# Performance work log

Measured on AMD Instinct MI355X. Metric: run time of the kernel, lower is better.

Reference implementation:

```python
import jax, jax.numpy as jnp
import numpy as np

MUL_S, MUL_V = 16, 8   # 16x0e + 8x1o -> input dim 16 + 8*3 = 40
N = 500_000
SQRT3 = 3.0 ** 0.5

# e3nn normalize2mom: scale act so E[act(x)^2]=1 for x~N(0,1)
def _norm2mom(act):
    xs = np.linspace(-12.0, 12.0, 200001)
    pdf = np.exp(-0.5 * xs * xs) / np.sqrt(2.0 * np.pi)
    m2 = np.trapz(act(xs) ** 2 * pdf, xs)
    return float(1.0 / np.sqrt(m2))

SILU_C = _norm2mom(lambda x: x / (1.0 + np.exp(-x)))
SIG_C = _norm2mom(lambda x: 1.0 / (1.0 + np.exp(-x)))

# e3nn path normalization (irrep_normalization='component', path_normalization='element')
C_SC = (1.0 / (MUL_S * MUL_S + MUL_V * MUL_V)) ** 0.5          # 0e outputs (scalars & gates)
C_V = (3.0 / (2 * MUL_S * MUL_V)) ** 0.5                        # 1o output (gated)


def setup_inputs() -> dict:
    key = jax.random.key(0)
    ks = jax.random.split(key, 7)
    return {
        "x": jax.random.normal(ks[0], (N, MUL_S + 3 * MUL_V), dtype=jnp.float32),
        "W_ss0": jax.random.normal(ks[1], (MUL_S, MUL_S, MUL_S), dtype=jnp.float32),
        "W_vv0": jax.random.normal(ks[2], (MUL_V, MUL_V, MUL_S), dtype=jnp.float32),
        "W_ss1": jax.random.normal(ks[3], (MUL_S, MUL_S, MUL_V), dtype=jnp.float32),
        "W_vv1": jax.random.normal(ks[4], (MUL_V, MUL_V, MUL_V), dtype=jnp.float32),
        "W_sv": jax.random.normal(ks[5], (MUL_S, MUL_V, MUL_V), dtype=jnp.float32),
        "W_vs": jax.random.normal(ks[6], (MUL_V, MUL_S, MUL_V), dtype=jnp.float32),
    }


def reference(x, W_ss0, W_vv0, W_ss1, W_vv1, W_sv, W_vs):
    # split irreps: scalars [N,16], vectors [N,8,3]
    s = x[:, :MUL_S]
    v = x[:, MUL_S:].reshape(-1, MUL_V, 3)

    # FullyConnectedTensorProduct(x, x) -> scalars(16x0e) + gates(8x0e) + gated(8x1o)
    # wigner_3j(0,0,0)=1 ; (1,1,0)=(0,1,1)=(1,0,1)=I/sqrt(3)
    scal = C_SC * (
        jnp.einsum('zu,zv,uvw->zw', s, s, W_ss0)
        + jnp.einsum('zui,zvi,uvw->zw', v, v, W_vv0) / SQRT3
    )
    gates_pre = C_SC * (
        jnp.einsum('zu,zv,uvw->zw', s, s, W_ss1)
        + jnp.einsum('zui,zvi,uvw->zw', v, v, W_vv1) / SQRT3
    )
    gated = (C_V / SQRT3) * (
        jnp.einsum('zu,zvi,uvw->zwi', s, v, W_sv)
        + jnp.einsum('zui,zv,uvw->zwi', v, s, W_vs)
    )

    # Gate: normalized silu on even scalars, normalized sigmoid gates * gated vectors
    out_s = SILU_C * jax.nn.silu(scal)                 # [N,16]
    g = SIG_C * jax.nn.sigmoid(gates_pre)              # [N,8]
    out_v = g[:, :, None] * gated                      # [N,8,3]
    return jnp.concatenate([out_s, out_v.reshape(-1, MUL_V * 3)], axis=1)
```

## Files before the change

kernel.cpp:

```cpp
#include <hip/hip_runtime.h>
#include <math.h>

#define NPTS 200001

typedef _Float16 f16;
typedef f16 f16x2 __attribute__((ext_vector_type(2)));
typedef f16 f16x8 __attribute__((ext_vector_type(8)));
typedef float f32x16 __attribute__((ext_vector_type(16)));

#define B1BYTES  21952
#define B2OFF    21952
#define BBYTES   24128
#define STAGEOFF 24128
#define LDSBYTES (24128 + 4*2560)

__global__ void prep(const float* __restrict__ wss0, const float* __restrict__ wvv0,
                     const float* __restrict__ wss1, const float* __restrict__ wvv1,
                     const float* __restrict__ wsv,  const float* __restrict__ wvs,
                     float* __restrict__ partials, f16* __restrict__ bpack)
{
    const int b = blockIdx.x;
    const int t = threadIdx.x;
    if (b < 4) {
        float ls = 0.f, lg = 0.f;
        for (int i = b * 256 + t; i < NPTS; i += 1024) {
            float xv  = -12.0f + 24.0f * ((float)i / 200000.0f);
            float pdf = __expf(-0.5f * xv * xv) * 0.39894228040143267794f;
            float sg  = 1.0f / (1.0f + __expf(-xv));
            float si  = xv * sg;
            float wt  = (i == 0 || i == NPTS - 1) ? 0.5f : 1.0f;
            ls = fmaf(wt * si * si, pdf, ls);
            lg = fmaf(wt * sg * sg, pdf, lg);
        }
        __shared__ float r1[256], r2[256];
        r1[t] = ls; r2[t] = lg;
        __syncthreads();
        for (int st = 128; st > 0; st >>= 1) {
            if (t < st) { r1[t] += r1[t + st]; r2[t] += r2[t + st]; }
            __syncthreads();
        }
        if (t == 0) { partials[b] = r1[0]; partials[4 + b] = r2[0]; }
    } else {
        const int gid = (b - 4) * 256 + t;
        const float CSC  = 0.05590169943749474241f;
        const float CSC3 = 0.05590169943749474241f / 1.7320508075688772935f;
        if (gid < 10976) {
            const int tk   = gid / 392;
            const int rem  = gid - tk * 392;
            const int unit = rem >> 3;
            const int j    = rem & 7;
            float val = 0.f;
            if (unit < 48) {
                const int hf  = (unit >= 24) ? 1 : 0;
                const int col = unit - 24 * hf;
                const int k   = tk * 16 + hf * 8 + j;
                if (k < 256) {
                    const int u = k >> 4, t16 = k & 15;
                    val = (col < 16) ? CSC * wss0[(u * 16 + t16) * 16 + col]
                                     : CSC * wss1[(u * 16 + t16) * 8 + (col - 16)];
                } else {
                    const int kk = k - 256;
                    const int r8 = (kk >> 3) & 7, c8 = kk & 7;
                    val = (col < 16) ? CSC3 * wvv0[(r8 * 8 + c8) * 16 + col]
                                     : CSC3 * wvv1[(r8 * 8 + c8) * 8 + (col - 16)];
                }
            }
            bpack[gid] = (f16)val;
        } else if (gid < 12064) {
            const int e    = gid - 10976;
            const int ks   = e / 136;
            const int rem  = e - ks * 136;
            const int unit = rem >> 3;
            const int j    = rem & 7;
            float val = 0.f;
            if (unit < 16) {
                const int hf = unit >> 3;
                const int w  = unit & 7;
                const int k  = ks * 16 + hf * 8 + j;
                const int a  = k >> 3, bb = k & 7;
                val = 0.0625f * (wsv[(a * 8 + bb) * 8 + w] + wvs[(bb * 16 + a) * 8 + w]);
            }
            bpack[gid] = (f16)val;
        }
    }
}

__global__ __launch_bounds__(256, 4) void seg_main(
    const float* __restrict__ x,
    const f16* __restrict__ bpack,
    const float* __restrict__ partials,
    float* __restrict__ out, int n, int nchunks)
{
    const int tid  = threadIdx.x;
    const int lane = tid & 63;
    const int wid  = tid >> 6;
    const int col  = lane & 31;
    const int hf   = lane >> 5;

    __shared__ float4 lds4[LDSBYTES / 16];
    {
        const float4* src = (const float4*)bpack;
#pragma unroll
        for (int i = 0; i < 6; ++i) {
            const int idx = i * 256 + tid;
            if (idx < BBYTES / 16) lds4[idx] = src[idx];
        }
    }
    __syncthreads();

    char* ldsc = (char*)lds4;
    const int uA = (col < 24) ? (hf * 24 + col) * 16 : 48 * 16;
    const int u0 = B2OFF + ((col >= 24) ? (hf * 8 + col - 24) * 16 : 256);
    const int u1 = B2OFF + ((col < 8)   ? (hf * 8 + col) * 16      : 256);
    const int u2 = B2OFF + ((col >= 8 && col < 16) ? (hf * 8 + col - 8) * 16 : 256);
    const f16x8* BA  = (const f16x8*)(ldsc + uA);
    const f16x8* B0p = (const f16x8*)(ldsc + u0);
    const f16x8* B1p = (const f16x8*)(ldsc + u1);
    const f16x8* B2p = (const f16x8*)(ldsc + u2);

    float*  stagef = (float*)(ldsc + STAGEOFF + wid * 2560);
    float4* stage4 = (float4*)(ldsc + STAGEOFF + wid * 2560);

    const int gsrc = 4 * (hf * 32 + 16 + (col & 7));
    const int vo   = 16 + (col & 7) * 3 + ((col < 8) ? 1 : ((col < 16) ? 2 : 0));
    const bool wrV = (col < 16) || (col >= 24);

    const float dx = 24.0f / 200000.0f;
    const float silu_c = rsqrtf((partials[0] + partials[1] + partials[2] + partials[3]) * dx);
    const float sig_c  = rsqrtf((partials[4] + partials[5] + partials[6] + partials[7]) * dx);

    const long long nf40 = (long long)n * 40;
    const int stride = gridDim.x * 4;

    for (int chunk = blockIdx.x * 4 + wid; chunk < nchunks; chunk += stride) {
        const int row  = chunk * 32 + col;
        const int lrow = (row < n) ? row : (n - 1);

        f16x2 s2[8];
        f16x2 vc[3][4];
        {
            const float4* p4 = (const float4*)(x + (size_t)lrow * 40);
            float4 q0 = p4[0], q1 = p4[1], q2 = p4[2], q3 = p4[3], q4 = p4[4];
            float4 q5 = p4[5], q6 = p4[6], q7 = p4[7], q8 = p4[8], q9 = p4[9];
            s2[0].x = (f16)q0.x; s2[0].y = (f16)q0.y;
            s2[1].x = (f16)q0.z; s2[1].y = (f16)q0.w;
            s2[2].x = (f16)q1.x; s2[2].y = (f16)q1.y;
            s2[3].x = (f16)q1.z; s2[3].y = (f16)q1.w;
            s2[4].x = (f16)q2.x; s2[4].y = (f16)q2.y;
            s2[5].x = (f16)q2.z; s2[5].y = (f16)q2.w;
            s2[6].x = (f16)q3.x; s2[6].y = (f16)q3.y;
            s2[7].x = (f16)q3.z; s2[7].y = (f16)q3.w;
            vc[0][0].x = (f16)q4.x; vc[0][0].y = (f16)q4.w;
            vc[1][0].x = (f16)q4.y; vc[1][0].y = (f16)q5.x;
            vc[2][0].x = (f16)q4.z; vc[2][0].y = (f16)q5.y;
            vc[0][1].x = (f16)q5.z; vc[0][1].y = (f16)q6.y;
            vc[1][1].x = (f16)q5.w; vc[1][1].y = (f16)q6.z;
            vc[2][1].x = (f16)q6.x; vc[2][1].y = (f16)q6.w;
            vc[0][2].x = (f16)q7.x; vc[0][2].y = (f16)q7.w;
            vc[1][2].x = (f16)q7.y; vc[1][2].y = (f16)q8.x;
            vc[2][2].x = (f16)q7.z; vc[2][2].y = (f16)q8.y;
            vc[0][3].x = (f16)q8.z; vc[0][3].y = (f16)q9.y;
            vc[1][3].x = (f16)q8.w; vc[1][3].y = (f16)q9.z;
            vc[2][3].x = (f16)q9.x; vc[2][3].y = (f16)q9.w;
        }

        f16x2 shp[4];
#pragma unroll
        for (int m = 0; m < 4; ++m) shp[m] = hf ? s2[4 + m] : s2[m];

        union { f16x2 h[4]; f16x8 v; } A;
        f32x16 accA, accB;
#pragma unroll
        for (int r = 0; r < 16; ++r) { accA[r] = 0.f; accB[r] = 0.f; }

#pragma unroll
        for (int t = 0; t < 16; ++t) {
            f16 sv = (t & 1) ? s2[t >> 1].y : s2[t >> 1].x;
            f16x2 su2; su2.x = sv; su2.y = sv;
#pragma unroll
            for (int m = 0; m < 4; ++m) A.h[m] = su2 * shp[m];
            accA = __builtin_amdgcn_mfma_f32_32x32x16_f16(A.v, BA[t * 49], accA, 0, 0, 0);
        }
#pragma unroll
        for (int tt = 0; tt < 12; ++tt) {
            const int i   = tt >> 2;
            const int ttm = tt & 3;
            f16x2 pr = vc[i][ttm];
            f16 sv = hf ? pr.y : pr.x;
            f16x2 su2; su2.x = sv; su2.y = sv;
#pragma unroll
            for (int m = 0; m < 4; ++m) A.h[m] = su2 * vc[i][m];
            accA = __builtin_amdgcn_mfma_f32_32x32x16_f16(A.v, BA[(16 + tt) * 49], accA, 0, 0, 0);
        }
#pragma unroll
        for (int ks = 0; ks < 8; ++ks) {
            f16x2 pr = s2[ks];
            f16 sv = hf ? pr.y : pr.x;
            f16x2 su2; su2.x = sv; su2.y = sv;
            union { f16x2 h[4]; f16x8 v; } A0, A1, A2;
#pragma unroll
            for (int m = 0; m < 4; ++m) {
                A0.h[m] = su2 * vc[0][m];
                A1.h[m] = su2 * vc[1][m];
                A2.h[m] = su2 * vc[2][m];
            }
            accA = __builtin_amdgcn_mfma_f32_32x32x16_f16(A0.v, B0p[ks * 17], accA, 0, 0, 0);
            accB = __builtin_amdgcn_mfma_f32_32x32x16_f16(A1.v, B1p[ks * 17], accB, 0, 0, 0);
            accB = __builtin_amdgcn_mfma_f32_32x32x16_f16(A2.v, B2p[ks * 17], accB, 0, 0, 0);
        }

#pragma unroll
        for (int half = 0; half < 2; ++half) {
#pragma unroll
            for (int rr = 0; rr < 8; ++rr) {
                const int r = half * 8 + rr;
                const float aval = accA[r];
                const float sgm  = 1.0f / (1.0f + __expf(-aval));
                const float gm   = __int_as_float(
                    __builtin_amdgcn_ds_bpermute(gsrc, __float_as_int(sig_c * sgm)));
                const int zloc = (((r & 3) + 8 * (r >> 2)) & 7) + 4 * hf + ((rr >> 2) << 3);
                if (col < 16) stagef[zloc * 40 + col] = silu_c * aval * sgm;
                if (wrV)      stagef[zloc * 40 + vo]  = gm * ((col < 16) ? accB[r] : aval);
            }
            if ((long long)(chunk * 32 + half * 16 + 15) < (long long)n) {
                float4* o4 = (float4*)out + (size_t)chunk * 320 + half * 160;
                float4 f0 = stage4[lane];
                float4 f1 = stage4[64 + lane];
                o4[lane]      = f0;
                o4[64 + lane] = f1;
                if (lane < 32) { float4 f2 = stage4[128 + lane]; o4[128 + lane] = f2; }
            } else {
#pragma unroll
                for (int k2 = 0; k2 < 3; ++k2) {
                    if (k2 == 2 && lane >= 32) break;
                    float4 fv = stage4[k2 * 64 + lane];
                    const long long fbase = (long long)chunk * 1280 + half * 640
                                          + (k2 * 64 + lane) * 4;
#pragma unroll
                    for (int e = 0; e < 4; ++e) {
                        const long long fi = fbase + e;
                        if (fi < nf40) out[fi] = ((const float*)&fv)[e];
                    }
                }
            }
        }
    }
}

extern "C" void kernel_launch(void* const* d_in, const int* in_sizes, int n_in,
                              void* d_out, int out_size, void* d_ws, size_t ws_size,
                              hipStream_t stream)
{
    (void)n_in; (void)out_size; (void)ws_size;
    const float* x    = (const float*)d_in[0];
    const float* wss0 = (const float*)d_in[1];
    const float* wvv0 = (const float*)d_in[2];
    const float* wss1 = (const float*)d_in[3];
    const float* wvv1 = (const float*)d_in[4];
    const float* wsv  = (const float*)d_in[5];
    const float* wvs  = (const float*)d_in[6];
    float* out = (float*)d_out;
    const int n = in_sizes[0] / 40;
    const int nchunks = (n + 31) / 32;

    char* ws = (char*)d_ws;
    float* partials = (float*)(ws + 0);
    f16*   bpack    = (f16*)(ws + 1024);

    int grid = (nchunks + 3) / 4;
    if (grid > 1024) grid = 1024;

    hipLaunchKernelGGL(prep, dim3(52), dim3(256), 0, stream,
                       wss0, wvv0, wss1, wvv1, wsv, wvs, partials, bpack);
    hipLaunchKernelGGL(seg_main, dim3(grid), dim3(256), 0, stream,
                       x, bpack, partials, out, n, nchunks);
}
```

Before: 190.0 us.

## Prefetch next chunk's input rows and pad LDS staging stride to 44

Loads the next chunk's 40-float input row into registers while the current chunk's MFMA work and epilogue run, a software-pipelined prefetch meant to hide global-load latency. It also pads the per-wave LDS staging buffer row stride from 40 to 44 floats to cut bank conflicts on the scattered epilogue writes, and changes the readback to index-remapped float4 reads. This holds ten extra float4 registers live across the loop, which may raise VGPR pressure and lower occupancy.

```diff
diff --git a/kernel.cpp b/kernel.cpp
--- a/kernel.cpp
+++ b/kernel.cpp
@@ -12,7 +12,7 @@
 #define B2OFF    21952
 #define BBYTES   24128
 #define STAGEOFF 24128
-#define LDSBYTES (24128 + 4*2560)
+#define LDSBYTES (24128 + 4*2816)
 
 __global__ void prep(const float* __restrict__ wss0, const float* __restrict__ wvv0,
                      const float* __restrict__ wss1, const float* __restrict__ wvv1,
@@ -118,8 +118,7 @@
     const f16x8* B1p = (const f16x8*)(ldsc + u1);
     const f16x8* B2p = (const f16x8*)(ldsc + u2);
 
-    float*  stagef = (float*)(ldsc + STAGEOFF + wid * 2560);
-    float4* stage4 = (float4*)(ldsc + STAGEOFF + wid * 2560);
+    float* stagef = (float*)(ldsc + STAGEOFF + wid * 2816);
 
     const int gsrc = 4 * (hf * 32 + 16 + (col & 7));
     const int vo   = 16 + (col & 7) * 3 + ((col < 8) ? 1 : ((col < 16) ? 2 : 0));
@@ -132,36 +131,49 @@
     const long long nf40 = (long long)n * 40;
     const int stride = gridDim.x * 4;
 
-    for (int chunk = blockIdx.x * 4 + wid; chunk < nchunks; chunk += stride) {
+    int chunk = blockIdx.x * 4 + wid;
+    float4 q0, q1, q2, q3, q4, q5, q6, q7, q8, q9;
+    if (chunk < nchunks) {
         const int row  = chunk * 32 + col;
         const int lrow = (row < n) ? row : (n - 1);
-
+        const float4* p4 = (const float4*)(x + (size_t)lrow * 40);
+        q0 = p4[0]; q1 = p4[1]; q2 = p4[2]; q3 = p4[3]; q4 = p4[4];
+        q5 = p4[5]; q6 = p4[6]; q7 = p4[7]; q8 = p4[8]; q9 = p4[9];
+    }
+
+    for (; chunk < nchunks; chunk += stride) {
         f16x2 s2[8];
         f16x2 vc[3][4];
+        s2[0].x = (f16)q0.x; s2[0].y = (f16)q0.y;
+        s2[1].x = (f16)q0.z; s2[1].y = (f16)q0.w;
+        s2[2].x = (f16)q1.x; s2[2].y = (f16)q1.y;
+        s2[3].x = (f16)q1.z; s2[3].y = (f16)q1.w;
+        s2[4].x = (f16)q2.x; s2[4].y = (f16)q2.y;
+        s2[5].x = (f16)q2.z; s2[5].y = (f16)q2.w;
+        s2[6].x = (f16)q3.x; s2[6].y = (f16)q3.y;
+        s2[7].x = (f16)q3.z; s2[7].y = (f16)q3.w;
+        vc[0][0].x = (f16)q4.x; vc[0][0].y = (f16)q4.w;
+        vc[1][0].x = (f16)q4.y; vc[1][0].y = (f16)q5.x;
+        vc[2][0].x = (f16)q4.z; vc[2][0].y = (f16)q5.y;
+        vc[0][1].x = (f16)q5.z; vc[0][1].y = (f16)q6.y;
+        vc[1][1].x = (f16)q5.w; vc[1][1].y = (f16)q6.z;
+        vc[2][1].x = (f16)q6.x; vc[2][1].y = (f16)q6.w;
+        vc[0][2].x = (f16)q7.x; vc[0][2].y = (f16)q7.w;
+        vc[1][2].x = (f16)q7.y; vc[1][2].y = (f16)q8.x;
+        vc[2][2].x = (f16)q7.z; vc[2][2].y = (f16)q8.y;
+        vc[0][3].x = (f16)q8.z; vc[0][3].y = (f16)q9.y;
+        vc[1][3].x = (f16)q8.w; vc[1][3].y = (f16)q9.z;
+        vc[2][3].x = (f16)q9.x; vc[2][3].y = (f16)q9.w;
+
         {
-            const float4* p4 = (const float4*)(x + (size_t)lrow * 40);
-            float4 q0 = p4[0], q1 = p4[1], q2 = p4[2], q3 = p4[3], q4 = p4[4];
-            float4 q5 = p4[5], q6 = p4[6], q7 = p4[7], q8 = p4[8], q9 = p4[9];
-            s2[0].x = (f16)q0.x; s2[0].y = (f16)q0.y;
-            s2[1].x = (f16)q0.z; s2[1].y = (f16)q0.w;
-            s2[2].x = (f16)q1.x; s2[2].y = (f16)q1.y;
-            s2[3].x = (f16)q1.z; s2[3].y = (f16)q1.w;
-            s2[4].x = (f16)q2.x; s2[4].y = (f16)q2.y;
-            s2[5].x = (f16)q2.z; s2[5].y = (f16)q2.w;
-            s2[6].x = (f16)q3.x; s2[6].y = (f16)q3.y;
-            s2[7].x = (f16)q3.z; s2[7].y = (f16)q3.w;
-            vc[0][0].x = (f16)q4.x; vc[0][0].y = (f16)q4.w;
-            vc[1][0].x = (f16)q4.y; vc[1][0].y = (f16)q5.x;
-            vc[2][0].x = (f16)q4.z; vc[2][0].y = (f16)q5.y;
-            vc[0][1].x = (f16)q5.z; vc[0][1].y = (f16)q6.y;
-            vc[1][1].x = (f16)q5.w; vc[1][1].y = (f16)q6.z;
-            vc[2][1].x = (f16)q6.x; vc[2][1].y = (f16)q6.w;
-            vc[0][2].x = (f16)q7.x; vc[0][2].y = (f16)q7.w;
-            vc[1][2].x = (f16)q7.y; vc[1][2].y = (f16)q8.x;
-            vc[2][2].x = (f16)q7.z; vc[2][2].y = (f16)q8.y;
-            vc[0][3].x = (f16)q8.z; vc[0][3].y = (f16)q9.y;
-            vc[1][3].x = (f16)q8.w; vc[1][3].y = (f16)q9.z;
-            vc[2][3].x = (f16)q9.x; vc[2][3].y = (f16)q9.w;
+            const int nxt = chunk + stride;
+            if (nxt < nchunks) {
+                const int row  = nxt * 32 + col;
+                const int lrow = (row < n) ? row : (n - 1);
+                const float4* p4 = (const float4*)(x + (size_t)lrow * 40);
+                q0 = p4[0]; q1 = p4[1]; q2 = p4[2]; q3 = p4[3]; q4 = p4[4];
+                q5 = p4[5]; q6 = p4[6]; q7 = p4[7]; q8 = p4[8]; q9 = p4[9];
+            }
         }
 
         f16x2 shp[4];
@@ -218,28 +230,31 @@
                 const float sgm  = 1.0f / (1.0f + __expf(-aval));
                 const float gm   = __int_as_float(
                     __builtin_amdgcn_ds_bpermute(gsrc, __float_as_int(sig_c * sgm)));
-                const int zloc = (((r & 3) + 8 * (r >> 2)) & 7) + 4 * hf + ((rr >> 2) << 3);
-                if (col < 16) stagef[zloc * 40 + col] = silu_c * aval * sgm;
-                if (wrV)      stagef[zloc * 40 + vo]  = gm * ((col < 16) ? accB[r] : aval);
-            }
-            if ((long long)(chunk * 32 + half * 16 + 15) < (long long)n) {
+                const int zloc = (rr & 3) + 8 * (rr >> 2) + 4 * hf;
+                if (col < 16) stagef[zloc * 44 + col] = silu_c * aval * sgm;
+                if (wrV)      stagef[zloc * 44 + vo]  = gm * ((col < 16) ? accB[r] : aval);
+            }
+            if (chunk * 32 + half * 16 + 15 < n) {
                 float4* o4 = (float4*)out + (size_t)chunk * 320 + half * 160;
-                float4 f0 = stage4[lane];
-                float4 f1 = stage4[64 + lane];
-                o4[lane]      = f0;
-                o4[64 + lane] = f1;
-                if (lane < 32) { float4 f2 = stage4[128 + lane]; o4[128 + lane] = f2; }
-            } else {
+                const float4* st4 = (const float4*)stagef;
 #pragma unroll
                 for (int k2 = 0; k2 < 3; ++k2) {
                     if (k2 == 2 && lane >= 32) break;
-                    float4 fv = stage4[k2 * 64 + lane];
-                    const long long fbase = (long long)chunk * 1280 + half * 640
-                                          + (k2 * 64 + lane) * 4;
+                    const int p  = k2 * 64 + lane;
+                    const int rw = p / 10, of = p - rw * 10;
+                    o4[p] = st4[rw * 11 + of];
+                }
+            } else {
+#pragma unroll
+                for (int k2 = 0; k2 < 3; ++k2) {
+                    if (k2 == 2 && lane >= 32) break;
+                    const int p = k2 * 64 + lane;
 #pragma unroll
                     for (int e = 0; e < 4; ++e) {
-                        const long long fi = fbase + e;
-                        if (fi < nf40) out[fi] = ((const float*)&fv)[e];
+                        const int  lf = p * 4 + e;
+                        const int  rw = lf / 40, of = lf - rw * 40;
+                        const long long fi = (long long)chunk * 1280 + half * 640 + lf;
+                        if (fi < nf40) out[fi] = stagef[rw * 44 + of];
                     }
                 }
             }
```

Result: slower. 248.3 us (+30.7%).
